# Optimization experiments

Hardware: AMD Instinct MI355X
Metric: run time of the kernel (lower is better)

The kernel has to match this reference:

```python
import jax, jax.numpy as jnp
import numpy as np

B, C, D = 4096, 128, 768
EPS = 1e-12
SEP = 4.0  # pair_dist in [0, 2], so 4.0 separates per-class key bands


def setup_inputs() -> dict:
    key = jax.random.key(0)
    k1, k2, k3, k4 = jax.random.split(key, 4)
    features = jax.random.normal(k1, (B, D), jnp.float32)
    centers = jax.random.normal(k2, (C, D), jnp.float32)
    labels = jax.random.randint(k3, (B,), 0, C, dtype=jnp.int32)
    cam_ids = jax.random.randint(k4, (B,), 0, 8, dtype=jnp.int32)
    return {"features": features, "centers": centers, "labels": labels, "cam_ids": cam_ids}


def _l2norm(x):
    return x / jnp.maximum(jnp.linalg.norm(x, axis=1, keepdims=True), EPS)


def reference(features, centers, labels, cam_ids):
    # cam_ids is unused by the original module.
    E = _l2norm(features)                         # [B, D] unit embeddings
    Cn = _l2norm(jax.lax.stop_gradient(centers))  # [C, D] unit centers (detached)

    S = E @ E.T                                   # [B, B] pairwise cosine (differentiable)
    EC = jnp.sum(E * Cn[labels], axis=1)          # [B] cosine(embedding_i, center_{label_i})

    li = labels[:, None]
    lj = labels[None, :]
    ar = jnp.arange(B)
    upper = ar[:, None] < ar[None, :]             # i < j (each unordered pair once)
    valid = (li == lj) & upper                    # within-class pairs

    # pair distances are computed under no_grad in torch -> stop_gradient
    pd = jax.lax.stop_gradient(1.0 - jnp.clip(S, -1.0, 1.0))  # [B, B]

    # per-class lower-median threshold via ONE global sort:
    # key = class_id * SEP + pair_dist groups pairs by class, sorted by dist within class
    m = jnp.zeros((C,), jnp.int32).at[labels].add(1)   # class sizes
    npairs = (m * (m - 1)) // 2                         # pairs per class
    key_mat = jnp.where(valid, li.astype(jnp.float32) * SEP + pd, jnp.inf)
    sorted_keys = jnp.sort(key_mat.ravel())             # [B*B]
    offs = jnp.cumsum(npairs) - npairs                  # start of each class segment
    med_idx = offs + jnp.maximum(npairs - 1, 0) // 2    # torch.median = lower median
    thr = sorted_keys[med_idx] - SEP * jnp.arange(C, dtype=jnp.float32)
    thr = jnp.where(npairs > 0, thr, jnp.inf)           # classes with <2 samples: no pairs

    sel = valid & (pd > thr[labels][:, None])           # strict > as in torch

    # random interpolation ratio (no_grad in torch)
    r = jax.lax.stop_gradient(jax.random.uniform(jax.random.key(1), (B, B), jnp.float32))

    # sampled = normalize(r*e_i + (1-r)*e_j); since ||e||=1:
    #   ||sampled_pre||^2 = r^2 + (1-r)^2 + 2 r (1-r) <e_i, e_j>
    #   <sampled, c> = (r <e_i,c> + (1-r) <e_j,c>) / ||sampled_pre||
    norm2 = r * r + (1.0 - r) * (1.0 - r) + 2.0 * r * (1.0 - r) * S
    norm = jnp.maximum(jnp.sqrt(jnp.maximum(norm2, 0.0)), EPS)
    dot = (r * EC[:, None] + (1.0 - r) * EC[None, :]) / norm
    dist = 1.0 - jnp.clip(dot, -1.0, 1.0)               # [B, B]

    # the torch loop iterates over every label occurrence, so a class with m_c
    # occurrences contributes its class loss (and pair count) m_c times
    w = m[labels].astype(jnp.float32)[:, None]          # weight per pair (left label's class)
    loss = jnp.sum(jnp.where(sel, w * dist, 0.0))
    nsamp = jnp.sum(jnp.where(sel, w, 0.0))
    return jnp.where(nsamp > 0, loss / nsamp, 0.0)
```

## Files before the change

### kernel.cpp

```cpp
#include <hip/hip_runtime.h>

#define B_ 4096
#define C_ 128
#define D_ 768
#define NT 1024
#define NW (NT/64)
#define M_MAX 96
#define P_MAX (M_MAX*(M_MAX-1)/2)
#define CK 128
#define NCH (D_/CK)
#define SROW 132
#define TILE_F (M_MAX*SROW)
#define LM2 2
#define RC 127
#define SPT ((M_MAX*(CK/4) + NT - 1)/NT)
#define LCAP 64
#define WS_SOFF 4096u
#define WS_SBYTES ((size_t)C_ * P_MAX * 4u)
#define WS_NEED (WS_SOFF + WS_SBYTES + (size_t)C_ * M_MAX * 4u)

__device__ __forceinline__ float wave_red(float v){
#pragma unroll
  for (int o = 32; o > 0; o >>= 1) v += __shfl_down(v, o, 64);
  return v;
}
__device__ __forceinline__ float clamp1(float x){ return fminf(fmaxf(x, -1.f), 1.f); }
__device__ __forceinline__ unsigned rotl32(unsigned x, int r){ return (x << r) | (x >> (32 - r)); }
__device__ __forceinline__ float dot4(float4 a, float4 b){
  return fmaf(a.x, b.x, fmaf(a.y, b.y, fmaf(a.z, b.z, a.w * b.w)));
}

__device__ float rand_ij(unsigned n){
  const unsigned half = (unsigned)B_ * (unsigned)B_ / 2u;
  unsigned c0, c1; bool hi;
  if (n < half){ c0 = n; c1 = n + half; hi = false; }
  else         { c0 = n - half; c1 = n; hi = true; }
  const unsigned K0 = 0u, K1 = 1u, K2 = 0x1BD11BDBu;
  unsigned x0 = c0 + K0, x1 = c1 + K1;
#define TFR(r) { x0 += x1; x1 = rotl32(x1, (r)); x1 ^= x0; }
  TFR(13) TFR(15) TFR(26) TFR(6)  x0 += K1; x1 += K2 + 1u;
  TFR(17) TFR(29) TFR(16) TFR(24) x0 += K2; x1 += K0 + 2u;
  TFR(13) TFR(15) TFR(26) TFR(6)  x0 += K0; x1 += K1 + 3u;
  TFR(17) TFR(29) TFR(16) TFR(24) x0 += K1; x1 += K2 + 4u;
  TFR(13) TFR(15) TFR(26) TFR(6)  x0 += K2; x1 += K0 + 5u;
#undef TFR
  unsigned bits = hi ? x1 : x0;
  return __uint_as_float((bits >> 9) | 0x3F800000u) - 1.0f;
}

__device__ __forceinline__ void decode_pair(int p, int m, int* a_, int* b_){
  float fm = (float)(2*m - 1);
  int a = (int)((fm - sqrtf(fm*fm - 8.0f*(float)p)) * 0.5f);
  a = max(0, min(a, m - 2));
  while (a > 0 && (a*(2*m - 1 - a))/2 > p) --a;
  while (((a + 1)*(2*m - 2 - a))/2 <= p) ++a;
  *a_ = a;
  *b_ = a + 1 + (p - (a*(2*m - 1 - a))/2);
}

__device__ float dotg(const float* x, const float* y){
  float s = 0.f;
  for (int k = 0; k < D_; ++k) s = fmaf(x[k], y[k], s);
  return s;
}
__device__ float S_pair_g(const float* feat, int ga, int gb){
  const float* ra = feat + (size_t)ga * D_;
  const float* rb = feat + (size_t)gb * D_;
  float d = dotg(ra, rb);
  float na = 1.f / fmaxf(sqrtf(dotg(ra, ra)), 1e-12f);
  float nb = 1.f / fmaxf(sqrtf(dotg(rb, rb)), 1e-12f);
  return d * na * nb;
}

__global__ __launch_bounds__(NT) void k_gram(
    const float* __restrict__ feat, const float* __restrict__ cent,
    const int* __restrict__ labels,
    float* __restrict__ wsS, float* __restrict__ wsE)
{
  const int c  = blockIdx.x >> 1;
  const int kh = blockIdx.x & 1;
  const int tid = threadIdx.x;

  __shared__ int   gid_s[M_MAX];
  __shared__ int   mcount;
  __shared__ __align__(16) float tile[2 * TILE_F];
  __shared__ __align__(16) float cvec[2][CK];
  __shared__ float selfs[M_MAX];
  __shared__ float ecs[M_MAX];
  __shared__ float cn_sh;

  if (tid == 0) mcount = 0;
  __syncthreads();
  {
    const int4* lab4 = (const int4*)labels;
    for (int i = tid; i < B_ / 4; i += NT){
      int4 L = lab4[i];
      int base = i << 2;
      if (L.x == c){ int p = atomicAdd(&mcount, 1); if (p < M_MAX) gid_s[p] = base; }
      if (L.y == c){ int p = atomicAdd(&mcount, 1); if (p < M_MAX) gid_s[p] = base + 1; }
      if (L.z == c){ int p = atomicAdd(&mcount, 1); if (p < M_MAX) gid_s[p] = base + 2; }
      if (L.w == c){ int p = atomicAdd(&mcount, 1); if (p < M_MAX) gid_s[p] = base + 3; }
    }
  }
  __syncthreads();
  const int m = mcount;
  if (m < 2 || m > M_MAX) return;

  const int nst = m * (CK / 4);
  float* wsc = wsS + (size_t)c * P_MAX;

  const int h    = (m + 1) >> 1;
  const int Upair = h * (h + 1) / 2;
  const int hec  = (m + 2) >> 1;
  const int U    = Upair + hec;

  int c0[LM2], c1[LM2], c2[LM2], c3[LM2];
  int tAv[LM2], tBv[LM2];
  float acc[LM2][4];
  int nlay = 0;
#pragma unroll
  for (int t = 0; t < LM2; ++t){
    acc[t][0] = acc[t][1] = acc[t][2] = acc[t][3] = 0.f;
    c0[t] = c1[t] = c2[t] = c3[t] = 0; tAv[t] = 0; tBv[t] = -3;
    int u = tid + t * NT;
    if (u < U){
      nlay = t + 1;
      if (u < Upair){
        int ta = 0;
        while ((ta + 1) * h - ((ta + 1) * ta) / 2 <= u) ++ta;
        int tb = ta + (u - (ta * h - (ta * (ta - 1)) / 2));
        if (ta == tb || (u & 1) == kh){
          c0[t] = ta; c1[t] = ta + h; c2[t] = tb; c3[t] = tb + h;
          tAv[t] = ta; tBv[t] = tb;
        }
      } else {
        int g = u - Upair;
        int l1 = g + hec;
        c0[t] = g;
        c1[t] = (l1 == m) ? RC : ((l1 < m) ? l1 : 0);
        c2[t] = RC; c3[t] = RC;
        tAv[t] = g; tBv[t] = -1;
      }
    }
  }

  float4 pf[SPT];
  float4 cpf;
#pragma unroll
  for (int k = 0; k < SPT; ++k){
    int e = tid + k * NT;
    if (e < nst){
      int r = e >> 5, j = e & 31;
      pf[k] = ((const float4*)(feat + (size_t)gid_s[r] * D_))[j];
    }
  }
  if (tid < CK/4) cpf = ((const float4*)(cent + (size_t)c * D_))[tid];
#pragma unroll
  for (int k = 0; k < SPT; ++k){
    int e = tid + k * NT;
    if (e < nst){
      int r = e >> 5, j = e & 31;
      ((float4*)&tile[r * SROW])[j] = pf[k];
    }
  }
  if (tid < CK/4) ((float4*)cvec[0])[tid] = cpf;
  __syncthreads();

  for (int ch = 0; ch < NCH; ++ch){
    const int cur = ch & 1;
    if (ch + 1 < NCH){
      const int d0 = (ch + 1) * CK;
#pragma unroll
      for (int k = 0; k < SPT; ++k){
        int e = tid + k * NT;
        if (e < nst){
          int r = e >> 5, j = e & 31;
          pf[k] = ((const float4*)(feat + (size_t)gid_s[r] * D_ + d0))[j];
        }
      }
      if (tid < CK/4) cpf = ((const float4*)(cent + (size_t)c * D_ + d0))[tid];
    }
    {
      const float* tl = tile + cur * TILE_F;
      const float4* cv4 = (const float4*)cvec[cur];
#pragma unroll
      for (int t = 0; t < LM2; ++t){
        if (t < nlay && tBv[t] != -3){
          const float4* A0 = (c0[t] == RC) ? cv4 : (const float4*)&tl[c0[t] * SROW];
          const float4* A1 = (c1[t] == RC) ? cv4 : (const float4*)&tl[c1[t] * SROW];
          const float4* Bp0 = (c2[t] == RC) ? cv4 : (const float4*)&tl[c2[t] * SROW];
          const float4* Bp1 = (c3[t] == RC) ? cv4 : (const float4*)&tl[c3[t] * SROW];
          float s00 = 0.f, s01 = 0.f, s10 = 0.f, s11 = 0.f;
#pragma unroll 8
          for (int j = 0; j < CK/4; ++j){
            float4 a0 = A0[j], a1 = A1[j], b0 = Bp0[j], b1 = Bp1[j];
            s00 += dot4(a0, b0); s01 += dot4(a0, b1);
            s10 += dot4(a1, b0); s11 += dot4(a1, b1);
          }
          acc[t][0] += s00; acc[t][1] += s01;
          acc[t][2] += s10; acc[t][3] += s11;
        }
      }
    }
    if (ch + 1 < NCH){
      float* tn = tile + (cur ^ 1) * TILE_F;
#pragma unroll
      for (int k = 0; k < SPT; ++k){
        int e = tid + k * NT;
        if (e < nst){
          int r = e >> 5, j = e & 31;
          ((float4*)&tn[r * SROW])[j] = pf[k];
        }
      }
      if (tid < CK/4) ((float4*)cvec[cur ^ 1])[tid] = cpf;
    }
    __syncthreads();
  }

#pragma unroll
  for (int t = 0; t < LM2; ++t){
    if (t < nlay && tBv[t] != -3){
      if (tBv[t] == -1){
        int g = tAv[t], l1 = g + hec;
        ecs[g] = acc[t][0];
        if (l1 == m) cn_sh = acc[t][2];
        else if (l1 < m) ecs[l1] = acc[t][2];
      } else {
        const int ta = tAv[t], tb = tBv[t];
        const int a1 = ta + h;
        if (ta == tb){
          if (ta < m) selfs[ta] = acc[t][0];
          if (a1 < m) selfs[a1] = acc[t][3];
        }
      }
    }
  }
  __syncthreads();
  if (tid < m){
    float rn  = 1.f / fmaxf(sqrtf(selfs[tid]), 1e-12f);
    float cno = 1.f / fmaxf(sqrtf(cn_sh), 1e-12f);
    selfs[tid] = rn;
    ecs[tid] = ecs[tid] * rn * cno;
  }
  __syncthreads();

#pragma unroll
  for (int t = 0; t < LM2; ++t){
    if (t < nlay && tBv[t] >= 0){
      const int ta = tAv[t], tb = tBv[t], a1 = ta + h, b1 = tb + h;
      const int  pa[4]  = { ta, ta, tb, a1 };
      const int  pb[4]  = { tb, b1, a1, b1 };
      const bool dif    = (ta != tb);
      const bool val[4] = { dif, b1 < m, dif && (a1 < m), dif && (a1 < m) && (b1 < m) };
#pragma unroll
      for (int s = 0; s < 4; ++s){
        if (val[s]){
          float S = acc[t][s] * selfs[pa[s]]; S *= selfs[pb[s]];
          int p = (pa[s] * (2*m - 1 - pa[s])) / 2 + (pb[s] - pa[s] - 1);
          wsc[p] = S;
        }
      }
    }
  }
  if (kh == 0 && tid < m) wsE[c * M_MAX + tid] = ecs[tid];
}

__global__ __launch_bounds__(NT) void k_sel(
    const float* __restrict__ feat, const float* __restrict__ cent,
    const int* __restrict__ labels,
    float* __restrict__ lossv, float* __restrict__ wv,
    unsigned* __restrict__ flags,
    const float* __restrict__ wsS, const float* __restrict__ wsE,
    float* __restrict__ out)
{
  const int c = blockIdx.x;
  const int tid = threadIdx.x;
  const int wid = tid >> 6, lane = tid & 63;

  __shared__ int   gid_s[M_MAX];
  __shared__ int   mcount;
  __shared__ float Sl[P_MAX];
  __shared__ unsigned short fidx_s[P_MAX];
  __shared__ float ecs[M_MAX];
  __shared__ int   wcnt[NW * 64];
  __shared__ int   B0_sh, ex_sh, B1_sh, ex2_sh;
  __shared__ float thr_sh;
  __shared__ float lst[LCAP];
  __shared__ int   listn;
  __shared__ float redbuf[2 * NW];
  __shared__ int   last_sh;

  if (tid == 0) mcount = 0;
  __syncthreads();
  {
    const int4* lab4 = (const int4*)labels;
    for (int i = tid; i < B_ / 4; i += NT){
      int4 L = lab4[i];
      int base = i << 2;
      if (L.x == c){ int p = atomicAdd(&mcount, 1); if (p < M_MAX) gid_s[p] = base; }
      if (L.y == c){ int p = atomicAdd(&mcount, 1); if (p < M_MAX) gid_s[p] = base + 1; }
      if (L.z == c){ int p = atomicAdd(&mcount, 1); if (p < M_MAX) gid_s[p] = base + 2; }
      if (L.w == c){ int p = atomicAdd(&mcount, 1); if (p < M_MAX) gid_s[p] = base + 3; }
    }
  }
  __syncthreads();
  const int m = mcount;

  float lloss = 0.f, lw = 0.f;

  if (m >= 2 && m <= M_MAX){
    const int P = m * (m - 1) / 2;
    const int k0 = (P - 1) >> 1;
    const float wc = (float)m;
    const float* wsc = wsS + (size_t)c * P_MAX;

    if (tid == 0) listn = 0;
    for (int p = tid; p < P; p += NT){
      float S = wsc[p];
      Sl[p] = S;
      float pd = 1.f - clamp1(S);
      fidx_s[p] = (unsigned short)min(4095, (int)(pd * 2048.f));
    }
    if (tid < m) ecs[tid] = wsE[c * M_MAX + tid];
    __syncthreads();

    const int nch = (P + NT - 1) / NT;
    int cl = 0;
    for (int t = 0; t < nch; ++t){
      int p = tid + t * NT;
      int bkt = -1;
      if (p < P) bkt = fidx_s[p] >> 6;
#pragma unroll
      for (int k = 0; k < 64; ++k){
        unsigned long long msk = __ballot(bkt == k);
        if (lane == k) cl += __popcll(msk);
      }
    }
    wcnt[wid*64 + lane] = cl;
    __syncthreads();
    if (tid < 64){
      int tot = 0;
#pragma unroll
      for (int w = 0; w < NW; ++w) tot += wcnt[w*64 + tid];
      int inc = tot;
#pragma unroll
      for (int o = 1; o < 64; o <<= 1){
        int v = __shfl_up(inc, o, 64);
        if (tid >= o) inc += v;
      }
      int excl = inc - tot;
      if (excl <= k0 && k0 < inc){ B0_sh = tid; ex_sh = excl; }
    }
    __syncthreads();
    const int Bsel0 = B0_sh;
    const int kt = k0 - ex_sh;
    cl = 0;
    for (int t = 0; t < nch; ++t){
      int p = tid + t * NT;
      int bkt = -1;
      if (p < P){
        int f = fidx_s[p];
        if ((f >> 6) == Bsel0) bkt = f & 63;
      }
#pragma unroll
      for (int k = 0; k < 64; ++k){
        unsigned long long msk = __ballot(bkt == k);
        if (lane == k) cl += __popcll(msk);
      }
    }
    wcnt[wid*64 + lane] = cl;
    __syncthreads();
    if (tid < 64){
      int tot = 0;
#pragma unroll
      for (int w = 0; w < NW; ++w) tot += wcnt[w*64 + tid];
      int inc = tot;
#pragma unroll
      for (int o = 1; o < 64; o <<= 1){
        int v = __shfl_up(inc, o, 64);
        if (tid >= o) inc += v;
      }
      int excl = inc - tot;
      if (excl <= kt && kt < inc){ B1_sh = tid; ex2_sh = excl; }
    }
    __syncthreads();
    const int fsel = (Bsel0 << 6) | B1_sh;
    const int ktf  = kt - ex2_sh;

    for (int p = tid; p < P; p += NT){
      if (fidx_s[p] == (unsigned short)fsel){
        int ix = atomicAdd(&listn, 1);
        if (ix < LCAP) lst[ix] = 1.f - clamp1(Sl[p]);
      }
    }
    __syncthreads();
    const int ln = listn;
    if (ln <= LCAP){
      if (tid < ln){
        float pdp = lst[tid];
        int lt = 0, eq = 0;
        for (int j = 0; j < ln; ++j){
          float v = lst[j];
          lt += (v < pdp); eq += (v == pdp);
        }
        if (lt <= ktf && ktf < lt + eq) thr_sh = pdp;
      }
    } else {
      for (int p = tid; p < P; p += NT){
        if (fidx_s[p] == (unsigned short)fsel){
          float pdp = 1.f - clamp1(Sl[p]);
          int lt = 0, eq = 0;
          for (int q = 0; q < P; ++q){
            float pdq = 1.f - clamp1(Sl[q]);
            lt += (pdq < pdp); eq += (pdq == pdp);
          }
          if (lt <= k0 && k0 < lt + eq) thr_sh = pdp;
        }
      }
    }
    __syncthreads();
    const float thr = thr_sh;

    for (int p = tid; p < P; p += NT){
      float S = Sl[p];
      float pd = 1.f - clamp1(S);
      if (pd > thr){
        int a, b; decode_pair(p, m, &a, &b);
        int ga = gid_s[a], gb = gid_s[b];
        float ea = ecs[a], eb = ecs[b];
        int i, j; float eci, ecj;
        if (ga < gb){ i = ga; j = gb; eci = ea; ecj = eb; }
        else        { i = gb; j = ga; eci = eb; ecj = ea; }
        float r = rand_ij((unsigned)i * (unsigned)B_ + (unsigned)j);
        float omr = 1.f - r;
        float n2 = r * r + omr * omr + 2.f * r * omr * S;
        float nrm = fmaxf(sqrtf(fmaxf(n2, 0.f)), 1e-12f);
        float dt = clamp1((r * eci + omr * ecj) / nrm);
        lloss += wc * (1.f - dt);
        lw += wc;
      }
    }
  } else if (m > M_MAX){
    int* mem = (int*)Sl;
    if (tid == 0) B0_sh = 0;
    __syncthreads();
    for (int i = tid; i < B_; i += NT)
      if (labels[i] == c){ int p = atomicAdd(&B0_sh, 1); mem[p] = i; }
    __syncthreads();
    const int P = m * (m - 1) / 2;
    const int k0 = (P - 1) >> 1;
    const float wc = (float)m;
    const float* cc = cent + (size_t)c * D_;
    const float cno = 1.f / fmaxf(sqrtf(dotg(cc, cc)), 1e-12f);
    for (int p = tid; p < P; p += NT){
      int a, b; decode_pair(p, m, &a, &b);
      float pdp = 1.f - clamp1(S_pair_g(feat, mem[a], mem[b]));
      int lt = 0, eq = 0;
      for (int q = 0; q < P; ++q){
        int a2, b2; decode_pair(q, m, &a2, &b2);
        float pdq = 1.f - clamp1(S_pair_g(feat, mem[a2], mem[b2]));
        lt += (pdq < pdp); eq += (pdq == pdp);
      }
      if (lt <= k0 && k0 < lt + eq) thr_sh = pdp;
    }
    __syncthreads();
    const float thr = thr_sh;
    for (int p = tid; p < P; p += NT){
      int a, b; decode_pair(p, m, &a, &b);
      int ga = mem[a], gb = mem[b];
      float S = S_pair_g(feat, ga, gb);
      float pd = 1.f - clamp1(S);
      if (pd > thr){
        if (ga > gb){ int t2 = ga; ga = gb; gb = t2; }
        const float* ra = feat + (size_t)ga * D_;
        const float* rb = feat + (size_t)gb * D_;
        float eci = dotg(ra, cc) / fmaxf(sqrtf(dotg(ra, ra)), 1e-12f) * cno;
        float ecj = dotg(rb, cc) / fmaxf(sqrtf(dotg(rb, rb)), 1e-12f) * cno;
        float r = rand_ij((unsigned)ga * (unsigned)B_ + (unsigned)gb);
        float omr = 1.f - r;
        float n2 = r * r + omr * omr + 2.f * r * omr * S;
        float nrm = fmaxf(sqrtf(fmaxf(n2, 0.f)), 1e-12f);
        float dt = clamp1((r * eci + omr * ecj) / nrm);
        lloss += wc * (1.f - dt);
        lw += wc;
      }
    }
  }

  lloss = wave_red(lloss); lw = wave_red(lw);
  if (lane == 0){ redbuf[wid] = lloss; redbuf[NW + wid] = lw; }
  __syncthreads();
  if (tid == 0){
    float tl = 0.f, tw = 0.f;
#pragma unroll
    for (int i = 0; i < NW; ++i){ tl += redbuf[i]; tw += redbuf[NW + i]; }
    __hip_atomic_store(&lossv[c], tl, __ATOMIC_RELAXED, __HIP_MEMORY_SCOPE_AGENT);
    __hip_atomic_store(&wv[c],   tw, __ATOMIC_RELAXED, __HIP_MEMORY_SCOPE_AGENT);
    unsigned old = __hip_atomic_fetch_add(&flags[0], 1u, __ATOMIC_ACQ_REL,
                                          __HIP_MEMORY_SCOPE_AGENT);
    last_sh = ((old & 127u) == 127u) ? 1 : 0;
  }
  __syncthreads();
  if (last_sh){
    float lv = 0.f, wvv = 0.f;
    if (tid < C_){
      lv  = __hip_atomic_load(&lossv[tid], __ATOMIC_RELAXED, __HIP_MEMORY_SCOPE_AGENT);
      wvv = __hip_atomic_load(&wv[tid],   __ATOMIC_RELAXED, __HIP_MEMORY_SCOPE_AGENT);
    }
    lv = wave_red(lv); wvv = wave_red(wvv);
    if (lane == 0){ redbuf[wid] = lv; redbuf[NW + wid] = wvv; }
    __syncthreads();
    if (tid == 0){
      float l = redbuf[0] + redbuf[1];
      float w = redbuf[NW] + redbuf[NW + 1];
      out[0] = (w > 0.f) ? (l / w) : 0.f;
    }
  }
}

__global__ __launch_bounds__(NT) void k_all(
    const float* __restrict__ feat, const float* __restrict__ cent,
    const int* __restrict__ labels,
    float* __restrict__ lossv, float* __restrict__ wv,
    unsigned* __restrict__ flags, float* __restrict__ out)
{
  const int c = blockIdx.x;
  const int tid = threadIdx.x;
  const int wid = tid >> 6, lane = tid & 63;

  __shared__ int   gid_s[M_MAX];
  __shared__ int   mcount;
  __shared__ __align__(16) float tile[2 * TILE_F];
  __shared__ __align__(16) float cvec[2][CK];
  float*          Sl     = tile;
  unsigned short* fidx_s = (unsigned short*)(tile + P_MAX);
  __shared__ float selfs[M_MAX];
  __shared__ float ecs[M_MAX];
  __shared__ float cn_sh;
  __shared__ int   wcnt[NW * 64];
  __shared__ int   B0_sh, ex_sh, B1_sh, ex2_sh;
  __shared__ float thr_sh;
  __shared__ float lst[LCAP];
  __shared__ int   listn;
  __shared__ float redbuf[2 * NW];
  __shared__ int   last_sh;

  if (tid == 0) mcount = 0;
  __syncthreads();
  {
    const int4* lab4 = (const int4*)labels;
    for (int i = tid; i < B_ / 4; i += NT){
      int4 L = lab4[i];
      int base = i << 2;
      if (L.x == c){ int p = atomicAdd(&mcount, 1); if (p < M_MAX) gid_s[p] = base; }
      if (L.y == c){ int p = atomicAdd(&mcount, 1); if (p < M_MAX) gid_s[p] = base + 1; }
      if (L.z == c){ int p = atomicAdd(&mcount, 1); if (p < M_MAX) gid_s[p] = base + 2; }
      if (L.w == c){ int p = atomicAdd(&mcount, 1); if (p < M_MAX) gid_s[p] = base + 3; }
    }
  }
  __syncthreads();
  const int m = mcount;

  float lloss = 0.f, lw = 0.f;

  if (m >= 2 && m <= M_MAX){
    const int P = m * (m - 1) / 2;
    const int k0 = (P - 1) >> 1;
    const float wc = (float)m;
    const int nst = m * (CK / 4);

    const int h    = (m + 1) >> 1;
    const int Upair = h * (h + 1) / 2;
    const int hec  = (m + 2) >> 1;
    const int U    = Upair + hec;

    int c0[LM2], c1[LM2], c2[LM2], c3[LM2];
    int tAv[LM2], tBv[LM2];
    float acc[LM2][4];
    int nlay = 0;
#pragma unroll
    for (int t = 0; t < LM2; ++t){
      acc[t][0] = acc[t][1] = acc[t][2] = acc[t][3] = 0.f;
      c0[t] = c1[t] = c2[t] = c3[t] = 0; tAv[t] = 0; tBv[t] = -3;
      int u = tid + t * NT;
      if (u < U){
        nlay = t + 1;
        if (u < Upair){
          int ta = 0;
          while ((ta + 1) * h - ((ta + 1) * ta) / 2 <= u) ++ta;
          int tb = ta + (u - (ta * h - (ta * (ta - 1)) / 2));
          c0[t] = ta; c1[t] = ta + h; c2[t] = tb; c3[t] = tb + h;
          tAv[t] = ta; tBv[t] = tb;
        } else {
          int g = u - Upair;
          int l1 = g + hec;
          c0[t] = g;
          c1[t] = (l1 == m) ? RC : ((l1 < m) ? l1 : 0);
          c2[t] = RC; c3[t] = RC;
          tAv[t] = g; tBv[t] = -1;
        }
      }
    }

    float4 pf[SPT];
    float4 cpf;
#pragma unroll
    for (int k = 0; k < SPT; ++k){
      int e = tid + k * NT;
      if (e < nst){
        int r = e >> 5, j = e & 31;
        pf[k] = ((const float4*)(feat + (size_t)gid_s[r] * D_))[j];
      }
    }
    if (tid < CK/4) cpf = ((const float4*)(cent + (size_t)c * D_))[tid];
#pragma unroll
    for (int k = 0; k < SPT; ++k){
      int e = tid + k * NT;
      if (e < nst){
        int r = e >> 5, j = e & 31;
        ((float4*)&tile[r * SROW])[j] = pf[k];
      }
    }
    if (tid < CK/4) ((float4*)cvec[0])[tid] = cpf;
    __syncthreads();

    for (int ch = 0; ch < NCH; ++ch){
      const int cur = ch & 1;
      if (ch + 1 < NCH){
        const int d0 = (ch + 1) * CK;
#pragma unroll
        for (int k = 0; k < SPT; ++k){
          int e = tid + k * NT;
          if (e < nst){
            int r = e >> 5, j = e & 31;
            pf[k] = ((const float4*)(feat + (size_t)gid_s[r] * D_ + d0))[j];
          }
        }
        if (tid < CK/4) cpf = ((const float4*)(cent + (size_t)c * D_ + d0))[tid];
      }
      {
        const float* tl = tile + cur * TILE_F;
        const float4* cv4 = (const float4*)cvec[cur];
#pragma unroll
        for (int t = 0; t < LM2; ++t){
          if (t < nlay){
            const float4* A0 = (c0[t] == RC) ? cv4 : (const float4*)&tl[c0[t] * SROW];
            const float4* A1 = (c1[t] == RC) ? cv4 : (const float4*)&tl[c1[t] * SROW];
            const float4* Bp0 = (c2[t] == RC) ? cv4 : (const float4*)&tl[c2[t] * SROW];
            const float4* Bp1 = (c3[t] == RC) ? cv4 : (const float4*)&tl[c3[t] * SROW];
            float s00 = 0.f, s01 = 0.f, s10 = 0.f, s11 = 0.f;
#pragma unroll 8
            for (int j = 0; j < CK/4; ++j){
              float4 a0 = A0[j], a1 = A1[j], b0 = Bp0[j], b1 = Bp1[j];
              s00 += dot4(a0, b0); s01 += dot4(a0, b1);
              s10 += dot4(a1, b0); s11 += dot4(a1, b1);
            }
            acc[t][0] += s00; acc[t][1] += s01;
            acc[t][2] += s10; acc[t][3] += s11;
          }
        }
      }
      if (ch + 1 < NCH){
        float* tn = tile + (cur ^ 1) * TILE_F;
#pragma unroll
        for (int k = 0; k < SPT; ++k){
          int e = tid + k * NT;
          if (e < nst){
            int r = e >> 5, j = e & 31;
            ((float4*)&tn[r * SROW])[j] = pf[k];
          }
        }
        if (tid < CK/4) ((float4*)cvec[cur ^ 1])[tid] = cpf;
      }
      __syncthreads();
    }

#pragma unroll
    for (int t = 0; t < LM2; ++t){
      if (t < nlay){
        if (tBv[t] == -1){
          int g = tAv[t], l1 = g + hec;
          ecs[g] = acc[t][0];
          if (l1 == m) cn_sh = acc[t][2];
          else if (l1 < m) ecs[l1] = acc[t][2];
        } else if (tBv[t] >= 0){
          const int ta = tAv[t], tb = tBv[t];
          const int a1 = ta + h;
          if (ta == tb){
            if (ta < m) selfs[ta] = acc[t][0];
            if (a1 < m) selfs[a1] = acc[t][3];
          }
        }
      }
    }
    __syncthreads();
    if (tid == 0) listn = 0;
    if (tid < m){
      float rn  = 1.f / fmaxf(sqrtf(selfs[tid]), 1e-12f);
      float cno = 1.f / fmaxf(sqrtf(cn_sh), 1e-12f);
      selfs[tid] = rn;
      ecs[tid] = ecs[tid] * rn * cno;
    }
    __syncthreads();

    float pdq_[LM2][4];
    int   fq_[LM2][4];
#pragma unroll
    for (int t = 0; t < LM2; ++t){
#pragma unroll
      for (int s = 0; s < 4; ++s){ pdq_[t][s] = 0.f; fq_[t][s] = -1; }
      if (t < nlay && tBv[t] >= 0){
        const int ta = tAv[t], tb = tBv[t], a1 = ta + h, b1 = tb + h;
        const int  pa[4]  = { ta, ta, tb, a1 };
        const int  pb[4]  = { tb, b1, a1, b1 };
        const bool dif    = (ta != tb);
        const bool val[4] = { dif, b1 < m, dif && (a1 < m), dif && (a1 < m) && (b1 < m) };
#pragma unroll
        for (int s = 0; s < 4; ++s){
          if (val[s]){
            float S = acc[t][s] * selfs[pa[s]]; S *= selfs[pb[s]];
            float pd = 1.f - clamp1(S);
            int p = (pa[s] * (2*m - 1 - pa[s])) / 2 + (pb[s] - pa[s] - 1);
            Sl[p] = S;
            int f = min(4095, (int)(pd * 2048.f));
            fidx_s[p] = (unsigned short)f;
            pdq_[t][s] = pd; fq_[t][s] = f;
          }
        }
      }
    }
    __syncthreads();

    const int nch = (P + NT - 1) / NT;
    int cl = 0;
    for (int t = 0; t < nch; ++t){
      int p = tid + t * NT;
      int bkt = -1;
      if (p < P) bkt = fidx_s[p] >> 6;
#pragma unroll
      for (int k = 0; k < 64; ++k){
        unsigned long long msk = __ballot(bkt == k);
        if (lane == k) cl += __popcll(msk);
      }
    }
    wcnt[wid*64 + lane] = cl;
    __syncthreads();
    if (tid < 64){
      int tot = 0;
#pragma unroll
      for (int w = 0; w < NW; ++w) tot += wcnt[w*64 + tid];
      int inc = tot;
#pragma unroll
      for (int o = 1; o < 64; o <<= 1){
        int v = __shfl_up(inc, o, 64);
        if (tid >= o) inc += v;
      }
      int excl = inc - tot;
      if (excl <= k0 && k0 < inc){ B0_sh = tid; ex_sh = excl; }
    }
    __syncthreads();
    const int Bsel0 = B0_sh;
    const int kt = k0 - ex_sh;
    cl = 0;
    for (int t = 0; t < nch; ++t){
      int p = tid + t * NT;
      int bkt = -1;
      if (p < P){
        int f = fidx_s[p];
        if ((f >> 6) == Bsel0) bkt = f & 63;
      }
#pragma unroll
      for (int k = 0; k < 64; ++k){
        unsigned long long msk = __ballot(bkt == k);
        if (lane == k) cl += __popcll(msk);
      }
    }
    wcnt[wid*64 + lane] = cl;
    __syncthreads();
    if (tid < 64){
      int tot = 0;
#pragma unroll
      for (int w = 0; w < NW; ++w) tot += wcnt[w*64 + tid];
      int inc = tot;
#pragma unroll
      for (int o = 1; o < 64; o <<= 1){
        int v = __shfl_up(inc, o, 64);
        if (tid >= o) inc += v;
      }
      int excl = inc - tot;
      if (excl <= kt && kt < inc){ B1_sh = tid; ex2_sh = excl; }
    }
    __syncthreads();
    const int fsel = (Bsel0 << 6) | B1_sh;
    const int ktf  = kt - ex2_sh;

#pragma unroll
    for (int t = 0; t < LM2; ++t){
#pragma unroll
      for (int s = 0; s < 4; ++s){
        if (fq_[t][s] == fsel){
          int ix = atomicAdd(&listn, 1);
          if (ix < LCAP) lst[ix] = pdq_[t][s];
        }
      }
    }
    __syncthreads();
    const int ln = listn;
    if (ln <= LCAP){
      if (tid < ln){
        float pdp = lst[tid];
        int lt = 0, eq = 0;
        for (int j = 0; j < ln; ++j){
          float v = lst[j];
          lt += (v < pdp); eq += (v == pdp);
        }
        if (lt <= ktf && ktf < lt + eq) thr_sh = pdp;
      }
    } else {
      for (int p = tid; p < P; p += NT){
        if (fidx_s[p] == (unsigned short)fsel){
          float pdp = 1.f - clamp1(Sl[p]);
          int lt = 0, eq = 0;
          for (int q = 0; q < P; ++q){
            float pdq = 1.f - clamp1(Sl[q]);
            lt += (pdq < pdp); eq += (pdq == pdp);
          }
          if (lt <= k0 && k0 < lt + eq) thr_sh = pdp;
        }
      }
    }
    __syncthreads();
    const float thr = thr_sh;

    for (int p = tid; p < P; p += NT){
      float S = Sl[p];
      float pd = 1.f - clamp1(S);
      if (pd > thr){
        int a, b; decode_pair(p, m, &a, &b);
        int ga = gid_s[a], gb = gid_s[b];
        float ea = ecs[a], eb = ecs[b];
        int i, j; float eci, ecj;
        if (ga < gb){ i = ga; j = gb; eci = ea; ecj = eb; }
        else        { i = gb; j = ga; eci = eb; ecj = ea; }
        float r = rand_ij((unsigned)i * (unsigned)B_ + (unsigned)j);
        float omr = 1.f - r;
        float n2 = r * r + omr * omr + 2.f * r * omr * S;
        float nrm = fmaxf(sqrtf(fmaxf(n2, 0.f)), 1e-12f);
        float dt = clamp1((r * eci + omr * ecj) / nrm);
        lloss += wc * (1.f - dt);
        lw += wc;
      }
    }
  } else if (m > M_MAX){
    int* mem = (int*)Sl;
    if (tid == 0) B0_sh = 0;
    __syncthreads();
    for (int i = tid; i < B_; i += NT)
      if (labels[i] == c){ int p = atomicAdd(&B0_sh, 1); mem[p] = i; }
    __syncthreads();
    const int P = m * (m - 1) / 2;
    const int k0 = (P - 1) >> 1;
    const float wc = (float)m;
    const float* cc = cent + (size_t)c * D_;
    const float cno = 1.f / fmaxf(sqrtf(dotg(cc, cc)), 1e-12f);
    for (int p = tid; p < P; p += NT){
      int a, b; decode_pair(p, m, &a, &b);
      float pdp = 1.f - clamp1(S_pair_g(feat, mem[a], mem[b]));
      int lt = 0, eq = 0;
      for (int q = 0; q < P; ++q){
        int a2, b2; decode_pair(q, m, &a2, &b2);
        float pdq = 1.f - clamp1(S_pair_g(feat, mem[a2], mem[b2]));
        lt += (pdq < pdp); eq += (pdq == pdp);
      }
      if (lt <= k0 && k0 < lt + eq) thr_sh = pdp;
    }
    __syncthreads();
    const float thr = thr_sh;
    for (int p = tid; p < P; p += NT){
      int a, b; decode_pair(p, m, &a, &b);
      int ga = mem[a], gb = mem[b];
      float S = S_pair_g(feat, ga, gb);
      float pd = 1.f - clamp1(S);
      if (pd > thr){
        if (ga > gb){ int t2 = ga; ga = gb; gb = t2; }
        const float* ra = feat + (size_t)ga * D_;
        const float* rb = feat + (size_t)gb * D_;
        float eci = dotg(ra, cc) / fmaxf(sqrtf(dotg(ra, ra)), 1e-12f) * cno;
        float ecj = dotg(rb, cc) / fmaxf(sqrtf(dotg(rb, rb)), 1e-12f) * cno;
        float r = rand_ij((unsigned)ga * (unsigned)B_ + (unsigned)gb);
        float omr = 1.f - r;
        float n2 = r * r + omr * omr + 2.f * r * omr * S;
        float nrm = fmaxf(sqrtf(fmaxf(n2, 0.f)), 1e-12f);
        float dt = clamp1((r * eci + omr * ecj) / nrm);
        lloss += wc * (1.f - dt);
        lw += wc;
      }
    }
  }

  lloss = wave_red(lloss); lw = wave_red(lw);
  if (lane == 0){ redbuf[wid] = lloss; redbuf[NW + wid] = lw; }
  __syncthreads();
  if (tid == 0){
    float tl = 0.f, tw = 0.f;
#pragma unroll
    for (int i = 0; i < NW; ++i){ tl += redbuf[i]; tw += redbuf[NW + i]; }
    __hip_atomic_store(&lossv[c], tl, __ATOMIC_RELAXED, __HIP_MEMORY_SCOPE_AGENT);
    __hip_atomic_store(&wv[c],   tw, __ATOMIC_RELAXED, __HIP_MEMORY_SCOPE_AGENT);
    unsigned old = __hip_atomic_fetch_add(&flags[0], 1u, __ATOMIC_ACQ_REL,
                                          __HIP_MEMORY_SCOPE_AGENT);
    last_sh = ((old & 127u) == 127u) ? 1 : 0;
  }
  __syncthreads();
  if (last_sh){
    float lv = 0.f, wvv = 0.f;
    if (tid < C_){
      lv  = __hip_atomic_load(&lossv[tid], __ATOMIC_RELAXED, __HIP_MEMORY_SCOPE_AGENT);
      wvv = __hip_atomic_load(&wv[tid],   __ATOMIC_RELAXED, __HIP_MEMORY_SCOPE_AGENT);
    }
    lv = wave_red(lv); wvv = wave_red(wvv);
    if (lane == 0){ redbuf[wid] = lv; redbuf[NW + wid] = wvv; }
    __syncthreads();
    if (tid == 0){
      float l = redbuf[0] + redbuf[1];
      float w = redbuf[NW] + redbuf[NW + 1];
      out[0] = (w > 0.f) ? (l / w) : 0.f;
    }
  }
}

extern "C" void kernel_launch(void* const* d_in, const int* in_sizes, int n_in,
                              void* d_out, int out_size, void* d_ws, size_t ws_size,
                              hipStream_t stream)
{
  const float* feat   = (const float*)d_in[0];
  const float* cent   = (const float*)d_in[1];
  const int*   labels = (const int*)d_in[2];

  char* ws = (char*)d_ws;
  float*    lossv = (float*)(ws + 0);
  float*    wvv   = (float*)(ws + 512);
  unsigned* flags = (unsigned*)(ws + 1024);
  float*    wsS   = (float*)(ws + WS_SOFF);
  float*    wsE   = (float*)(ws + WS_SOFF + WS_SBYTES);

  if (ws_size >= WS_NEED){
    k_gram<<<2 * C_, NT, 0, stream>>>(feat, cent, labels, wsS, wsE);
    k_sel<<<C_, NT, 0, stream>>>(feat, cent, labels, lossv, wvv, flags,
                                 wsS, wsE, (float*)d_out);
  } else {
    k_all<<<C_, NT, 0, stream>>>(feat, cent, labels, lossv, wvv, flags,
                                 (float*)d_out);
  }
}
```

Baseline: 116.9 us.

## Balance gram work across block halves and pass class membership to selection kernel

k_gram now splits only the off-diagonal tile pairs between the two blocks of a class, and each thread handles at most one work unit instead of a two-layer loop. Diagonal units are computed by both halves because both need self-norms. k_gram also writes class counts and member indices to workspace, so k_sel no longer rescans all labels with shared atomics. This removes a label scan in the second kernel and lowers per-thread register and control overhead, at the cost of a bit of extra global traffic and redundant diagonal work.

Measured after the change: 124.1 us. +6.1%, slower.

```diff
diff --git a/kernel.cpp b/kernel.cpp
--- a/kernel.cpp
+++ b/kernel.cpp
@@ -15,7 +15,9 @@
 #define RC 127
 #define SPT ((M_MAX*(CK/4) + NT - 1)/NT)
 #define LCAP 64
-#define WS_SOFF 4096u
+#define WS_MOFF 2048u
+#define WS_GOFF 2560u
+#define WS_SOFF 65536u
 #define WS_SBYTES ((size_t)C_ * P_MAX * 4u)
 #define WS_NEED (WS_SOFF + WS_SBYTES + (size_t)C_ * M_MAX * 4u)
 
@@ -75,6 +77,7 @@
 __global__ __launch_bounds__(NT) void k_gram(
     const float* __restrict__ feat, const float* __restrict__ cent,
     const int* __restrict__ labels,
+    int* __restrict__ wsM, int* __restrict__ wsG,
     float* __restrict__ wsS, float* __restrict__ wsE)
 {
   const int c  = blockIdx.x >> 1;
@@ -104,45 +107,46 @@
   }
   __syncthreads();
   const int m = mcount;
+  if (kh == 0 && tid == 0) wsM[c] = m;
   if (m < 2 || m > M_MAX) return;
+  if (kh == 0 && tid < m) wsG[c * M_MAX + tid] = gid_s[tid];
 
   const int nst = m * (CK / 4);
   float* wsc = wsS + (size_t)c * P_MAX;
 
   const int h    = (m + 1) >> 1;
-  const int Upair = h * (h + 1) / 2;
+  const int nOff = h * (h - 1) / 2;
+  const int half0 = (nOff + 1) >> 1;
+  const int qbase = (kh == 0) ? 0 : half0;
+  const int qcnt  = (kh == 0) ? half0 : (nOff - half0);
   const int hec  = (m + 2) >> 1;
-  const int U    = Upair + hec;
-
-  int c0[LM2], c1[LM2], c2[LM2], c3[LM2];
-  int tAv[LM2], tBv[LM2];
-  float acc[LM2][4];
-  int nlay = 0;
-#pragma unroll
-  for (int t = 0; t < LM2; ++t){
-    acc[t][0] = acc[t][1] = acc[t][2] = acc[t][3] = 0.f;
-    c0[t] = c1[t] = c2[t] = c3[t] = 0; tAv[t] = 0; tBv[t] = -3;
-    int u = tid + t * NT;
-    if (u < U){
-      nlay = t + 1;
-      if (u < Upair){
-        int ta = 0;
-        while ((ta + 1) * h - ((ta + 1) * ta) / 2 <= u) ++ta;
-        int tb = ta + (u - (ta * h - (ta * (ta - 1)) / 2));
-        if (ta == tb || (u & 1) == kh){
-          c0[t] = ta; c1[t] = ta + h; c2[t] = tb; c3[t] = tb + h;
-          tAv[t] = ta; tBv[t] = tb;
-        }
-      } else {
-        int g = u - Upair;
-        int l1 = g + hec;
-        c0[t] = g;
-        c1[t] = (l1 == m) ? RC : ((l1 < m) ? l1 : 0);
-        c2[t] = RC; c3[t] = RC;
-        tAv[t] = g; tBv[t] = -1;
-      }
-    }
-  }
+  const int U    = qcnt + h + hec;
+
+  int uty = -1;
+  int ta_ = 0, tb_ = 0, g_ = 0;
+  int rc0 = 0, rc1 = 0, rc2 = 0, rc3 = 0;
+  if (tid < U){
+    if (tid < qcnt){
+      int q = qbase + tid;
+      int ta = 0;
+      while ((ta + 1) * (2*h - 2 - ta) / 2 <= q) ++ta;
+      int tb = ta + 1 + (q - (ta * (2*h - 1 - ta)) / 2);
+      uty = 0; ta_ = ta; tb_ = tb;
+      rc0 = ta; rc1 = ta + h; rc2 = tb; rc3 = tb + h;
+    } else if (tid < qcnt + h){
+      int d = tid - qcnt;
+      uty = 1; ta_ = d;
+      rc0 = d; rc1 = d + h; rc2 = d; rc3 = d + h;
+    } else {
+      int g = tid - qcnt - h;
+      int l1 = g + hec;
+      uty = 2; g_ = g;
+      rc0 = g;
+      rc1 = (l1 == m) ? RC : ((l1 < m) ? l1 : 0);
+      rc2 = RC; rc3 = RC;
+    }
+  }
+  float a0s = 0.f, a1s = 0.f, a2s = 0.f, a3s = 0.f;
 
   float4 pf[SPT];
   float4 cpf;
@@ -180,27 +184,21 @@
       }
       if (tid < CK/4) cpf = ((const float4*)(cent + (size_t)c * D_ + d0))[tid];
     }
-    {
+    if (uty >= 0){
       const float* tl = tile + cur * TILE_F;
       const float4* cv4 = (const float4*)cvec[cur];
-#pragma unroll
-      for (int t = 0; t < LM2; ++t){
-        if (t < nlay && tBv[t] != -3){
-          const float4* A0 = (c0[t] == RC) ? cv4 : (const float4*)&tl[c0[t] * SROW];
-          const float4* A1 = (c1[t] == RC) ? cv4 : (const float4*)&tl[c1[t] * SROW];
-          const float4* Bp0 = (c2[t] == RC) ? cv4 : (const float4*)&tl[c2[t] * SROW];
-          const float4* Bp1 = (c3[t] == RC) ? cv4 : (const float4*)&tl[c3[t] * SROW];
-          float s00 = 0.f, s01 = 0.f, s10 = 0.f, s11 = 0.f;
+      const float4* A0 = (rc0 == RC) ? cv4 : (const float4*)&tl[rc0 * SROW];
+      const float4* A1 = (rc1 == RC) ? cv4 : (const float4*)&tl[rc1 * SROW];
+      const float4* Bp0 = (rc2 == RC) ? cv4 : (const float4*)&tl[rc2 * SROW];
+      const float4* Bp1 = (rc3 == RC) ? cv4 : (const float4*)&tl[rc3 * SROW];
+      float s00 = 0.f, s01 = 0.f, s10 = 0.f, s11 = 0.f;
 #pragma unroll 8
-          for (int j = 0; j < CK/4; ++j){
-            float4 a0 = A0[j], a1 = A1[j], b0 = Bp0[j], b1 = Bp1[j];
-            s00 += dot4(a0, b0); s01 += dot4(a0, b1);
-            s10 += dot4(a1, b0); s11 += dot4(a1, b1);
-          }
-          acc[t][0] += s00; acc[t][1] += s01;
-          acc[t][2] += s10; acc[t][3] += s11;
-        }
-      }
+      for (int j = 0; j < CK/4; ++j){
+        float4 a0 = A0[j], a1 = A1[j], b0 = Bp0[j], b1 = Bp1[j];
+        s00 += dot4(a0, b0); s01 += dot4(a0, b1);
+        s10 += dot4(a1, b0); s11 += dot4(a1, b1);
+      }
+      a0s += s00; a1s += s01; a2s += s10; a3s += s11;
     }
     if (ch + 1 < NCH){
       float* tn = tile + (cur ^ 1) * TILE_F;
@@ -217,23 +215,14 @@
     __syncthreads();
   }
 
-#pragma unroll
-  for (int t = 0; t < LM2; ++t){
-    if (t < nlay && tBv[t] != -3){
-      if (tBv[t] == -1){
-        int g = tAv[t], l1 = g + hec;
-        ecs[g] = acc[t][0];
-        if (l1 == m) cn_sh = acc[t][2];
-        else if (l1 < m) ecs[l1] = acc[t][2];
-      } else {
-        const int ta = tAv[t], tb = tBv[t];
-        const int a1 = ta + h;
-        if (ta == tb){
-          if (ta < m) selfs[ta] = acc[t][0];
-          if (a1 < m) selfs[a1] = acc[t][3];
-        }
-      }
-    }
+  if (uty == 1){
+    selfs[ta_] = a0s;
+    if (ta_ + h < m) selfs[ta_ + h] = a3s;
+  } else if (uty == 2){
+    ecs[g_] = a0s;
+    int l1 = g_ + hec;
+    if (l1 == m) cn_sh = a2s;
+    else if (l1 < m) ecs[l1] = a2s;
   }
   __syncthreads();
   if (tid < m){
@@ -244,22 +233,29 @@
   }
   __syncthreads();
 
-#pragma unroll
-  for (int t = 0; t < LM2; ++t){
-    if (t < nlay && tBv[t] >= 0){
-      const int ta = tAv[t], tb = tBv[t], a1 = ta + h, b1 = tb + h;
-      const int  pa[4]  = { ta, ta, tb, a1 };
-      const int  pb[4]  = { tb, b1, a1, b1 };
-      const bool dif    = (ta != tb);
-      const bool val[4] = { dif, b1 < m, dif && (a1 < m), dif && (a1 < m) && (b1 < m) };
-#pragma unroll
-      for (int s = 0; s < 4; ++s){
-        if (val[s]){
-          float S = acc[t][s] * selfs[pa[s]]; S *= selfs[pb[s]];
-          int p = (pa[s] * (2*m - 1 - pa[s])) / 2 + (pb[s] - pa[s] - 1);
-          wsc[p] = S;
-        }
-      }
+  if (uty == 0){
+    const int a1r = ta_ + h, b1r = tb_ + h;
+    {
+      float S = a0s * selfs[ta_]; S *= selfs[tb_];
+      wsc[(ta_*(2*m - 1 - ta_))/2 + (tb_ - ta_ - 1)] = S;
+    }
+    if (b1r < m){
+      float S = a1s * selfs[ta_]; S *= selfs[b1r];
+      wsc[(ta_*(2*m - 1 - ta_))/2 + (b1r - ta_ - 1)] = S;
+    }
+    if (a1r < m){
+      float S = a2s * selfs[tb_]; S *= selfs[a1r];
+      wsc[(tb_*(2*m - 1 - tb_))/2 + (a1r - tb_ - 1)] = S;
+    }
+    if (a1r < m && b1r < m){
+      float S = a3s * selfs[a1r]; S *= selfs[b1r];
+      wsc[(a1r*(2*m - 1 - a1r))/2 + (b1r - a1r - 1)] = S;
+    }
+  } else if (uty == 1){
+    const int d = ta_, l1 = ta_ + h;
+    if (l1 < m){
+      float S = a1s * selfs[d]; S *= selfs[l1];
+      wsc[(d*(2*m - 1 - d))/2 + (l1 - d - 1)] = S;
     }
   }
   if (kh == 0 && tid < m) wsE[c * M_MAX + tid] = ecs[tid];
@@ -270,6 +266,7 @@
     const int* __restrict__ labels,
     float* __restrict__ lossv, float* __restrict__ wv,
     unsigned* __restrict__ flags,
+    const int* __restrict__ wsM, const int* __restrict__ wsG,
     const float* __restrict__ wsS, const float* __restrict__ wsE,
     float* __restrict__ out)
 {
@@ -278,7 +275,6 @@
   const int wid = tid >> 6, lane = tid & 63;
 
   __shared__ int   gid_s[M_MAX];
-  __shared__ int   mcount;
   __shared__ float Sl[P_MAX];
   __shared__ unsigned short fidx_s[P_MAX];
   __shared__ float ecs[M_MAX];
@@ -290,21 +286,7 @@
   __shared__ float redbuf[2 * NW];
   __shared__ int   last_sh;
 
-  if (tid == 0) mcount = 0;
-  __syncthreads();
-  {
-    const int4* lab4 = (const int4*)labels;
-    for (int i = tid; i < B_ / 4; i += NT){
-      int4 L = lab4[i];
-      int base = i << 2;
-      if (L.x == c){ int p = atomicAdd(&mcount, 1); if (p < M_MAX) gid_s[p] = base; }
-      if (L.y == c){ int p = atomicAdd(&mcount, 1); if (p < M_MAX) gid_s[p] = base + 1; }
-      if (L.z == c){ int p = atomicAdd(&mcount, 1); if (p < M_MAX) gid_s[p] = base + 2; }
-      if (L.w == c){ int p = atomicAdd(&mcount, 1); if (p < M_MAX) gid_s[p] = base + 3; }
-    }
-  }
-  __syncthreads();
-  const int m = mcount;
+  const int m = wsM[c];
 
   float lloss = 0.f, lw = 0.f;
 
@@ -315,13 +297,16 @@
     const float* wsc = wsS + (size_t)c * P_MAX;
 
     if (tid == 0) listn = 0;
+    if (tid < m){
+      gid_s[tid] = wsG[c * M_MAX + tid];
+      ecs[tid]   = wsE[c * M_MAX + tid];
+    }
     for (int p = tid; p < P; p += NT){
       float S = wsc[p];
       Sl[p] = S;
       float pd = 1.f - clamp1(S);
       fidx_s[p] = (unsigned short)min(4095, (int)(pd * 2048.f));
     }
-    if (tid < m) ecs[tid] = wsE[c * M_MAX + tid];
     __syncthreads();
 
     const int nch = (P + NT - 1) / NT;
@@ -941,13 +926,15 @@
   float*    lossv = (float*)(ws + 0);
   float*    wvv   = (float*)(ws + 512);
   unsigned* flags = (unsigned*)(ws + 1024);
+  int*      wsM   = (int*)(ws + WS_MOFF);
+  int*      wsG   = (int*)(ws + WS_GOFF);
   float*    wsS   = (float*)(ws + WS_SOFF);
   float*    wsE   = (float*)(ws + WS_SOFF + WS_SBYTES);
 
   if (ws_size >= WS_NEED){
-    k_gram<<<2 * C_, NT, 0, stream>>>(feat, cent, labels, wsS, wsE);
+    k_gram<<<2 * C_, NT, 0, stream>>>(feat, cent, labels, wsM, wsG, wsS, wsE);
     k_sel<<<C_, NT, 0, stream>>>(feat, cent, labels, lossv, wvv, flags,
-                                 wsS, wsE, (float*)d_out);
+                                 wsM, wsG, wsS, wsE, (float*)d_out);
   } else {
     k_all<<<C_, NT, 0, stream>>>(feat, cent, labels, lossv, wvv, flags,
                                  (float*)d_out);
```
